# Kernel optimization log

Measured on AMD Instinct MI355X. Metric: run time of the kernel, lower is better.

## Reference

```python
import jax, jax.numpy as jnp
import numpy as np

N_NODES = 100000
N_EDGES = 600000
N_FEAT = 128
N_HID = 128
N_GRAPHS = 256


def gcn_conv(x, src, dst, W, b, n_nodes):
    # PyG GCNConv: h = x @ W; add self-loops; sym-normalize; scatter-add; + bias
    h = x @ W  # [N, H]
    loop = jnp.arange(n_nodes)
    s = jnp.concatenate([src, loop])
    d = jnp.concatenate([dst, loop])
    deg = jax.ops.segment_sum(jnp.ones_like(d, dtype=h.dtype), d, num_segments=n_nodes)
    dinv = jnp.where(deg > 0, jax.lax.rsqrt(deg), 0.0)
    norm = dinv[s] * dinv[d]  # [E+N]
    msg = h[s] * norm[:, None]  # gather + scale
    out = jax.ops.segment_sum(msg, d, num_segments=n_nodes)  # scatter-add
    return out + b


def setup_inputs() -> dict:
    key = jax.random.key(0)
    ks = jax.random.split(key, 12)
    x = jax.random.normal(ks[0], (N_NODES, N_FEAT), dtype=jnp.float32)
    edge_index = jax.random.randint(ks[1], (2, N_EDGES), 0, N_NODES, dtype=jnp.int64)
    batch = jnp.sort(jax.random.randint(ks[2], (N_NODES,), 0, N_GRAPHS, dtype=jnp.int64))
    def lin(k, fi, fo):
        s = 1.0 / np.sqrt(fi)
        return jax.random.uniform(k, (fi, fo), jnp.float32, -s, s)
    params = {
        'W1': lin(ks[3], N_FEAT, N_HID), 'b1': jnp.zeros((N_HID,), jnp.float32),
        'W2': lin(ks[4], N_HID, N_HID), 'b2': jnp.zeros((N_HID,), jnp.float32),
        'W3': lin(ks[5], N_HID, N_HID), 'b3': jnp.zeros((N_HID,), jnp.float32),
        'W4': lin(ks[6], N_HID, N_HID), 'b4': jnp.zeros((N_HID,), jnp.float32),
        'Ws1': lin(ks[7], N_HID, N_HID), 'bs1': jnp.zeros((N_HID,), jnp.float32),
        'Ws2': lin(ks[8], N_HID, 1), 'bs2': jnp.zeros((1,), jnp.float32),
    }
    return {'x': x, 'edge_index': edge_index, 'batch': batch, **params}


def reference(x, edge_index, batch, W1, b1, W2, b2, W3, b3, W4, b4, Ws1, bs1, Ws2, bs2):
    src, dst = edge_index[0], edge_index[1]
    h = x
    # 2 conv blocks = 4 GCNConv layers, each followed by ReLU
    for W, b in ((W1, b1), (W2, b2), (W3, b3), (W4, b4)):
        h = jax.nn.relu(gcn_conv(h, src, dst, W, b, N_NODES))
    # global mean pool over nodes per graph
    sums = jax.ops.segment_sum(h, batch, num_segments=N_GRAPHS)  # [G, H]
    cnt = jax.ops.segment_sum(jnp.ones((h.shape[0],), h.dtype), batch, num_segments=N_GRAPHS)
    pooled = sums / jnp.maximum(cnt, 1.0)[:, None]
    # summary MLP: Linear -> ReLU -> Linear(->1)
    out = jax.nn.relu(pooled @ Ws1 + bs1) @ Ws2 + bs2  # [G, 1]
    return out
```

## Files before the change

kernel.cpp:

```cpp
#include <hip/hip_runtime.h>

#define N_NODES 100000
#define N_EDGES 600000
#define NF 128
#define NG 256

typedef _Float16 f16;
typedef f16 half8 __attribute__((ext_vector_type(8)));
typedef f16 half4v __attribute__((ext_vector_type(4)));
typedef float float4v __attribute__((ext_vector_type(4)));


__global__ void k_count(const int* __restrict__ ei, int* __restrict__ counts) {
    int e = blockIdx.x * 256 + threadIdx.x;
    if (e < N_EDGES) atomicAdd(&counts[ei[N_EDGES + e]], 1);
}

__global__ void k_scan1(const int* __restrict__ counts, int* __restrict__ row_ptr,
                        int* __restrict__ bsums, float* __restrict__ dinv) {
    __shared__ int s[256];
    int b = blockIdx.x, t = threadIdx.x;
    int base = b * 2048 + t * 8;
    int local[8];
    int sum = 0;
#pragma unroll
    for (int q = 0; q < 8; q++) {
        int idx = base + q;
        int v = (idx < N_NODES) ? counts[idx] : 0;
        if (idx < N_NODES) dinv[idx] = 1.0f / sqrtf((float)(v + 1));
        local[q] = sum;
        sum += v;
    }
    s[t] = sum;
    __syncthreads();
    for (int off = 1; off < 256; off <<= 1) {
        int v = 0;
        if (t >= off) v = s[t - off];
        __syncthreads();
        s[t] += v;
        __syncthreads();
    }
    int excl = s[t] - sum;
#pragma unroll
    for (int q = 0; q < 8; q++) {
        int idx = base + q;
        if (idx < N_NODES) row_ptr[idx] = excl + local[q];
    }
    if (t == 255) bsums[b] = s[255];
}

__global__ void k_scan3(int* __restrict__ row_ptr, const int* __restrict__ bsums,
                        int* __restrict__ cursor) {
    __shared__ int pre;
    if (threadIdx.x == 0) {
        int g = blockIdx.x >> 3;
        int s = 0;
        for (int j = 0; j < g; j++) s += bsums[j];
        pre = s;
    }
    __syncthreads();
    int i = blockIdx.x * 256 + threadIdx.x;
    if (i < N_NODES) {
        int v = row_ptr[i] + pre;
        row_ptr[i] = v;
        cursor[i] = v;
        if (i == 0) row_ptr[N_NODES] = N_EDGES;
    }
}

__global__ void k_fill(const int* __restrict__ ei, int* __restrict__ cursor,
                       int* __restrict__ col,
                       const float* __restrict__ W1, const float* __restrict__ W2,
                       const float* __restrict__ W3, const float* __restrict__ W4,
                       f16* __restrict__ wtH) {
    int e = blockIdx.x * 256 + threadIdx.x;
    if (e < N_EDGES) {
        int d = ei[N_EDGES + e];
        int p = atomicAdd(&cursor[d], 1);
        col[p] = ei[e];
    }
    if (blockIdx.x < 256) {
        int idx = blockIdx.x * 256 + threadIdx.x;
        int layer = idx >> 14;
        int rem = idx & 16383;
        int j = rem & 7;
        int lane = (rem >> 3) & 63;
        int chunk = rem >> 9;
        int wave = chunk >> 3;
        int s = (chunk >> 1) & 3;
        int ct = chunk & 1;
        int n = wave * 32 + ct * 16 + (lane & 15);
        int k = s * 32 + (lane >> 4) * 8 + j;
        const float* W = (layer == 0) ? W1 : (layer == 1) ? W2 : (layer == 2) ? W3 : W4;
        wtH[layer * 16384 + rem] = (f16)W[k * NF + n];
    }
}


template <int XIN>
__global__ __launch_bounds__(256) void k_gemm_mfma(
    const float* __restrict__ X, const f16* __restrict__ A,
    const f16* __restrict__ WTH,
    f16* __restrict__ Z, int M) {
    __shared__ __align__(16) f16 As[64 * 136];

    const int t = threadIdx.x;
    const int row0 = blockIdx.x * 64;
    const int wave = t >> 6;
    const int lane = t & 63;
    const int nl = lane & 15;
    const int quad = lane >> 4;

    auto bofs = [&](int s, int ct) {
        return (size_t)((((wave * 8 + s * 2 + ct) * 64) + lane) << 3);
    };

    half8 cbh[2];
    cbh[0] = *(const half8*)(WTH + bofs(0, 0));
    cbh[1] = *(const half8*)(WTH + bofs(0, 1));

    if (XIN) {
#pragma unroll
        for (int q = 0; q < 8; q++) {
            int lin = t + q * 256;
            int r = lin >> 5, c4 = lin & 31;
            float4 v = make_float4(0.f, 0.f, 0.f, 0.f);
            if (row0 + r < M) v = ((const float4*)(X + (size_t)(row0 + r) * NF))[c4];
            half4v hv = {(f16)v.x, (f16)v.y, (f16)v.z, (f16)v.w};
            *(half4v*)&As[r * 136 + c4 * 4] = hv;
        }
    } else {
#pragma unroll
        for (int q = 0; q < 4; q++) {
            int lin = t + q * 256;
            int r = lin >> 4, c8 = lin & 15;
            half8 v = {};
            if (row0 + r < M) v = *(const half8*)(A + (size_t)(row0 + r) * NF + c8 * 8);
            *(half8*)&As[r * 136 + c8 * 8] = v;
        }
    }
    __syncthreads();

    float4v acc[2][4];
#pragma unroll
    for (int ct = 0; ct < 2; ct++)
#pragma unroll
        for (int rt = 0; rt < 4; rt++) acc[ct][rt] = (float4v)0.f;

#pragma unroll
    for (int s = 0; s < 4; s++) {
        half8 nbh[2];
        if (s < 3) {
            nbh[0] = *(const half8*)(WTH + bofs(s + 1, 0));
            nbh[1] = *(const half8*)(WTH + bofs(s + 1, 1));
        }
        half8 fa[4];
#pragma unroll
        for (int rt = 0; rt < 4; rt++)
            fa[rt] = *(half8*)&As[(rt * 16 + nl) * 136 + s * 32 + quad * 8];
#pragma unroll
        for (int ct = 0; ct < 2; ct++)
#pragma unroll
            for (int rt = 0; rt < 4; rt++)
                acc[ct][rt] = __builtin_amdgcn_mfma_f32_16x16x32_f16(fa[rt], cbh[ct], acc[ct][rt], 0, 0, 0);
        if (s < 3) {
            cbh[0] = nbh[0]; cbh[1] = nbh[1];
        }
    }

    __syncthreads();
#pragma unroll
    for (int ct = 0; ct < 2; ct++)
#pragma unroll
        for (int rt = 0; rt < 4; rt++)
#pragma unroll
            for (int r = 0; r < 4; r++)
                As[(rt * 16 + quad * 4 + r) * 136 + wave * 32 + ct * 16 + nl] =
                    (f16)acc[ct][rt][r];
    __syncthreads();
#pragma unroll
    for (int q = 0; q < 4; q++) {
        int lin = t + q * 256;
        int r = lin >> 4, c8 = lin & 15;
        if (row0 + r < M)
            *(half8*)(Z + (size_t)(row0 + r) * NF + c8 * 8) = *(half8*)&As[r * 136 + c8 * 8];
    }
}


#define ACHUNK 4

__global__ __launch_bounds__(256) void k_agg(const f16* __restrict__ z,
                                             const float* __restrict__ dinv,
                                             const int* __restrict__ row_ptr,
                                             const int* __restrict__ col,
                                             const float* __restrict__ bias,
                                             f16* __restrict__ h) {
    const int t = threadIdx.x;
    const int slot = t >> 4;
    const int fl = t & 15;
    const int sbase = (t & 48);
    const int n0 = (blockIdx.x * 16 + slot) * ACHUNK;
    const half8* z8 = (const half8*)z;

    float bb[8];
    {
        float4 b0 = ((const float4*)bias)[fl * 2];
        float4 b1 = ((const float4*)bias)[fl * 2 + 1];
        bb[0] = b0.x; bb[1] = b0.y; bb[2] = b0.z; bb[3] = b0.w;
        bb[4] = b1.x; bb[5] = b1.y; bb[6] = b1.z; bb[7] = b1.w;
    }

    for (int n = n0; n < n0 + ACHUNK && n < N_NODES; n++) {
        const float di = dinv[n];
        const int beg = row_ptr[n];
        const int end = row_ptr[n + 1];

        float acc[8];
        {
            half8 v = z8[(size_t)n * 16 + fl];
            float w = di * di;
#pragma unroll
            for (int j = 0; j < 8; j++) acc[j] = bb[j] + (float)v[j] * w;
        }

        for (int c = beg; c < end; c += 16) {
            int mcnt = end - c; if (mcnt > 16) mcnt = 16;
            int ce = c + fl;
            int colv = (ce < end) ? col[ce] : 0;
            float dvv = dinv[colv];

            int j = 0;
            for (; j + 1 < mcnt; j += 2) {
                int s1 = __shfl(colv, sbase + j, 64);
                float w1 = __shfl(dvv, sbase + j, 64) * di;
                int s2 = __shfl(colv, sbase + j + 1, 64);
                float w2 = __shfl(dvv, sbase + j + 1, 64) * di;
                half8 v1 = z8[(size_t)s1 * 16 + fl];
                half8 v2 = z8[(size_t)s2 * 16 + fl];
#pragma unroll
                for (int q = 0; q < 8; q++) acc[q] += (float)v1[q] * w1;
#pragma unroll
                for (int q = 0; q < 8; q++) acc[q] += (float)v2[q] * w2;
            }
            if (j < mcnt) {
                int s1 = __shfl(colv, sbase + j, 64);
                float w1 = __shfl(dvv, sbase + j, 64) * di;
                half8 v1 = z8[(size_t)s1 * 16 + fl];
#pragma unroll
                for (int q = 0; q < 8; q++) acc[q] += (float)v1[q] * w1;
            }
        }

        half8 o;
#pragma unroll
        for (int j = 0; j < 8; j++) o[j] = (f16)fmaxf(acc[j], 0.f);
        ((half8*)h)[(size_t)n * 16 + fl] = o;
    }
}


__global__ __launch_bounds__(256) void k_agg_gemm(
    const f16* __restrict__ z, const float* __restrict__ dinv,
    const int* __restrict__ row_ptr, const int* __restrict__ col,
    const float* __restrict__ bias,
    const f16* __restrict__ WTH,
    f16* __restrict__ Zout) {
    __shared__ __align__(16) f16 As[64 * 136];

    const int t = threadIdx.x;
    const int slot = t >> 4;
    const int fl = t & 15;
    const int sbase = (t & 48);
    const int n0 = (blockIdx.x * 16 + slot) * ACHUNK;
    const half8* z8 = (const half8*)z;

    float bb[8];
    {
        float4 b0 = ((const float4*)bias)[fl * 2];
        float4 b1 = ((const float4*)bias)[fl * 2 + 1];
        bb[0] = b0.x; bb[1] = b0.y; bb[2] = b0.z; bb[3] = b0.w;
        bb[4] = b1.x; bb[5] = b1.y; bb[6] = b1.z; bb[7] = b1.w;
    }

#pragma unroll 1
    for (int i = 0; i < ACHUNK; i++) {
        const int n = n0 + i;
        half8 o = {};
        if (n < N_NODES) {
            const float di = dinv[n];
            const int beg = row_ptr[n];
            const int end = row_ptr[n + 1];

            float acc[8];
            {
                half8 v = z8[(size_t)n * 16 + fl];
                float w = di * di;
#pragma unroll
                for (int j = 0; j < 8; j++) acc[j] = bb[j] + (float)v[j] * w;
            }

            for (int c = beg; c < end; c += 16) {
                int mcnt = end - c; if (mcnt > 16) mcnt = 16;
                int ce = c + fl;
                int colv = (ce < end) ? col[ce] : 0;
                float dvv = dinv[colv];

                int j = 0;
                for (; j + 1 < mcnt; j += 2) {
                    int s1 = __shfl(colv, sbase + j, 64);
                    float w1 = __shfl(dvv, sbase + j, 64) * di;
                    int s2 = __shfl(colv, sbase + j + 1, 64);
                    float w2 = __shfl(dvv, sbase + j + 1, 64) * di;
                    half8 v1 = z8[(size_t)s1 * 16 + fl];
                    half8 v2 = z8[(size_t)s2 * 16 + fl];
#pragma unroll
                    for (int q = 0; q < 8; q++) acc[q] += (float)v1[q] * w1;
#pragma unroll
                    for (int q = 0; q < 8; q++) acc[q] += (float)v2[q] * w2;
                }
                if (j < mcnt) {
                    int s1 = __shfl(colv, sbase + j, 64);
                    float w1 = __shfl(dvv, sbase + j, 64) * di;
                    half8 v1 = z8[(size_t)s1 * 16 + fl];
#pragma unroll
                    for (int q = 0; q < 8; q++) acc[q] += (float)v1[q] * w1;
                }
            }
#pragma unroll
            for (int j = 0; j < 8; j++) o[j] = (f16)fmaxf(acc[j], 0.f);
        }
        *(half8*)&As[(slot * ACHUNK + i) * 136 + fl * 8] = o;
    }

    const int wave = t >> 6;
    const int lane = t & 63;
    const int nl = lane & 15;
    const int quad = lane >> 4;
    const int row0 = blockIdx.x * 64;

    auto bofs = [&](int s, int ct) {
        return (size_t)((((wave * 8 + s * 2 + ct) * 64) + lane) << 3);
    };

    half8 cbh[2];
    cbh[0] = *(const half8*)(WTH + bofs(0, 0));
    cbh[1] = *(const half8*)(WTH + bofs(0, 1));
    __syncthreads();

    float4v acc[2][4];
#pragma unroll
    for (int ct = 0; ct < 2; ct++)
#pragma unroll
        for (int rt = 0; rt < 4; rt++) acc[ct][rt] = (float4v)0.f;

#pragma unroll
    for (int s = 0; s < 4; s++) {
        half8 nbh[2];
        if (s < 3) {
            nbh[0] = *(const half8*)(WTH + bofs(s + 1, 0));
            nbh[1] = *(const half8*)(WTH + bofs(s + 1, 1));
        }
        half8 fa[4];
#pragma unroll
        for (int rt = 0; rt < 4; rt++)
            fa[rt] = *(half8*)&As[(rt * 16 + nl) * 136 + s * 32 + quad * 8];
#pragma unroll
        for (int ct = 0; ct < 2; ct++)
#pragma unroll
            for (int rt = 0; rt < 4; rt++)
                acc[ct][rt] = __builtin_amdgcn_mfma_f32_16x16x32_f16(fa[rt], cbh[ct], acc[ct][rt], 0, 0, 0);
        if (s < 3) {
            cbh[0] = nbh[0]; cbh[1] = nbh[1];
        }
    }

    __syncthreads();
#pragma unroll
    for (int ct = 0; ct < 2; ct++)
#pragma unroll
        for (int rt = 0; rt < 4; rt++)
#pragma unroll
            for (int r = 0; r < 4; r++)
                As[(rt * 16 + quad * 4 + r) * 136 + wave * 32 + ct * 16 + nl] =
                    (f16)acc[ct][rt][r];
    __syncthreads();
#pragma unroll
    for (int q = 0; q < 4; q++) {
        int lin = t + q * 256;
        int r = lin >> 4, c8 = lin & 15;
        if (row0 + r < N_NODES)
            *(half8*)(Zout + (size_t)(row0 + r) * NF + c8 * 8) = *(half8*)&As[r * 136 + c8 * 8];
    }
}


#define POOL_CHUNK 64

__global__ __launch_bounds__(128) void k_pool2(const f16* __restrict__ h,
                                               const int* __restrict__ batch,
                                               float* __restrict__ pooled) {
    int f = threadIdx.x;
    int n0 = blockIdx.x * POOL_CHUNK;
    int n1 = n0 + POOL_CHUNK;
    if (n1 > N_NODES) n1 = N_NODES;
    if (n0 >= N_NODES) return;
    int g = batch[n0];
    float acc = 0.f;
    for (int n = n0; n < n1; n++) {
        int gn = batch[n];
        if (gn != g) {
            atomicAdd(&pooled[g * NF + f], acc);
            acc = 0.f;
            g = gn;
        }
        acc += (float)h[(size_t)n * NF + f];
    }
    atomicAdd(&pooled[g * NF + f], acc);
}


__global__ void k_mlp(const float* __restrict__ pooled, const int* __restrict__ batch,
                      const float* __restrict__ Ws1, const float* __restrict__ bs1,
                      const float* __restrict__ Ws2, const float* __restrict__ bs2,
                      float* __restrict__ out) {
    __shared__ float row[NF];
    __shared__ float red[NF];
    int g = blockIdx.x, f = threadIdx.x;
    int lo = 0, hi = N_NODES;
    while (lo < hi) { int mid = (lo + hi) >> 1; if (batch[mid] < g) lo = mid + 1; else hi = mid; }
    int start = lo;
    hi = N_NODES;
    while (lo < hi) { int mid = (lo + hi) >> 1; if (batch[mid] < g + 1) lo = mid + 1; else hi = mid; }
    float cnt = (float)(lo - start);
    row[f] = pooled[g * NF + f] / fmaxf(cnt, 1.f);
    __syncthreads();
    float t = bs1[f];
    for (int k = 0; k < NF; k++) t += row[k] * Ws1[k * NF + f];
    t = fmaxf(t, 0.f);
    red[f] = t * Ws2[f];
    __syncthreads();
    for (int s = 64; s > 0; s >>= 1) {
        if (f < s) red[f] += red[f + s];
        __syncthreads();
    }
    if (f == 0) out[g] = red[0] + bs2[0];
}


extern "C" void kernel_launch(void* const* d_in, const int* in_sizes, int n_in,
                              void* d_out, int out_size, void* d_ws, size_t ws_size,
                              hipStream_t stream) {
    const float* x    = (const float*)d_in[0];
    const int*   ei   = (const int*)d_in[1];
    const int*   batch= (const int*)d_in[2];
    const float* W1 = (const float*)d_in[3];  const float* b1 = (const float*)d_in[4];
    const float* W2 = (const float*)d_in[5];  const float* b2 = (const float*)d_in[6];
    const float* W3 = (const float*)d_in[7];  const float* b3 = (const float*)d_in[8];
    const float* W4 = (const float*)d_in[9];  const float* b4 = (const float*)d_in[10];
    const float* Ws1= (const float*)d_in[11]; const float* bs1= (const float*)d_in[12];
    const float* Ws2= (const float*)d_in[13]; const float* bs2= (const float*)d_in[14];
    float* out = (float*)d_out;

    char* ws = (char*)d_ws;
    size_t off = 0;
    auto alloc = [&](size_t bytes) {
        void* p = ws + off;
        off += (bytes + 255) & ~(size_t)255;
        return p;
    };
    f16*   bufA   = (f16*)alloc((size_t)N_NODES * NF * 2);
    f16*   bufB   = (f16*)alloc((size_t)N_NODES * NF * 2);
    f16*   wtH    = (f16*)alloc((size_t)4 * NF * NF * 2);
    int*   counts = (int*)alloc((size_t)N_NODES * 4);
    int*   row_ptr= (int*)alloc((size_t)(N_NODES + 1) * 4);
    int*   cursor = (int*)alloc((size_t)N_NODES * 4);
    int*   col    = (int*)alloc((size_t)N_EDGES * 4);
    int*   bsums  = (int*)alloc(64 * 4);
    float* dinv   = (float*)alloc((size_t)N_NODES * 4);
    float* pooled = (float*)alloc((size_t)NG * NF * 4);

    hipMemsetAsync(counts, 0, (size_t)N_NODES * 4, stream);
    hipMemsetAsync(pooled, 0, (size_t)NG * NF * 4, stream);
    k_count<<<(N_EDGES + 255) / 256, 256, 0, stream>>>(ei, counts);
    int nscan = (N_NODES + 2047) / 2048;
    k_scan1<<<nscan, 256, 0, stream>>>(counts, row_ptr, bsums, dinv);
    k_scan3<<<(N_NODES + 255) / 256, 256, 0, stream>>>(row_ptr, bsums, cursor);
    k_fill<<<(N_EDGES + 255) / 256, 256, 0, stream>>>(ei, cursor, col,
                                                      W1, W2, W3, W4, wtH);

    int gblocks = (N_NODES + 63) / 64;
    int ablocks = (N_NODES + 16 * ACHUNK - 1) / (16 * ACHUNK);

    k_gemm_mfma<1><<<gblocks, 256, 0, stream>>>(x, nullptr, wtH, bufA, N_NODES);
    k_agg_gemm<<<gblocks, 256, 0, stream>>>(bufA, dinv, row_ptr, col, b1,
                                            wtH + 16384, bufB);
    k_agg_gemm<<<gblocks, 256, 0, stream>>>(bufB, dinv, row_ptr, col, b2,
                                            wtH + 32768, bufA);
    k_agg_gemm<<<gblocks, 256, 0, stream>>>(bufA, dinv, row_ptr, col, b3,
                                            wtH + 49152, bufB);
    k_agg<<<ablocks, 256, 0, stream>>>(bufB, dinv, row_ptr, col, b4, bufA);

    int pblocks = (N_NODES + POOL_CHUNK - 1) / POOL_CHUNK;
    k_pool2<<<pblocks, 128, 0, stream>>>(bufA, batch, pooled);
    k_mlp<<<NG, 128, 0, stream>>>(pooled, batch, Ws1, bs1, Ws2, bs2, out);
}
```

Before: 368.5 us.

## Pre-scale GEMM outputs by dinv and interleave two-node neighbor gathers

Folds the source-side dinv factor into the GEMM epilogue, so the aggregation becomes a plain sum of prescaled rows times the destination dinv. This removes the per-edge dinv gather and multiply. The aggregation loop is restructured to prefetch row pointers, self rows and the first column chunk for all four nodes, then processes two nodes at once with up to four outstanding gathers each, raising memory-level parallelism. The cost is more registers and more branchy code, and the output is rounded to fp16 after the dinv scaling.

```diff
diff --git a/kernel.cpp b/kernel.cpp
--- a/kernel.cpp
+++ b/kernel.cpp
@@ -97,12 +97,110 @@
 }
 
 
-template <int XIN>
-__global__ __launch_bounds__(256) void k_gemm_mfma(
-    const float* __restrict__ X, const f16* __restrict__ A,
-    const f16* __restrict__ WTH,
-    f16* __restrict__ Z, int M) {
+__device__ __forceinline__ void agg_tail(const half8* __restrict__ z8,
+                                         const int* __restrict__ col,
+                                         int sbase, int fl, int beg, int end,
+                                         float acc[8]) {
+    for (int c = beg + 16; c < end; c += 16) {
+        int ce = c + fl;
+        int cv = (ce < end) ? col[ce] : 0;
+        int mc = end - c; if (mc > 16) mc = 16;
+        for (int j = 0; j < mc; j += 4) {
+            int kk = mc - j;
+            half8 v0 = {}, v1 = {}, v2 = {}, v3 = {};
+            int s0 = __shfl(cv, sbase + j + 0, 64);
+            v0 = z8[(size_t)s0 * 16 + fl];
+            if (kk > 1) { int s1 = __shfl(cv, sbase + j + 1, 64); v1 = z8[(size_t)s1 * 16 + fl]; }
+            if (kk > 2) { int s2 = __shfl(cv, sbase + j + 2, 64); v2 = z8[(size_t)s2 * 16 + fl]; }
+            if (kk > 3) { int s3 = __shfl(cv, sbase + j + 3, 64); v3 = z8[(size_t)s3 * 16 + fl]; }
+#pragma unroll
+            for (int q = 0; q < 8; q++) acc[q] += (float)v0[q];
+            if (kk > 1) {
+#pragma unroll
+                for (int q = 0; q < 8; q++) acc[q] += (float)v1[q];
+            }
+            if (kk > 2) {
+#pragma unroll
+                for (int q = 0; q < 8; q++) acc[q] += (float)v2[q];
+            }
+            if (kk > 3) {
+#pragma unroll
+                for (int q = 0; q < 8; q++) acc[q] += (float)v3[q];
+            }
+        }
+    }
+}
+
+__device__ __forceinline__ void agg_pair(const half8* __restrict__ z8,
+                                         const int* __restrict__ col,
+                                         int sbase, int fl,
+                                         int begA, int endA, int begB, int endB,
+                                         int colvA, int colvB,
+                                         float accA[8], float accB[8]) {
+    int mA = endA - begA; if (mA > 16) mA = 16;
+    int mB = endB - begB; if (mB > 16) mB = 16;
+    const int mmax = (mA > mB) ? mA : mB;
+    for (int j = 0; j < mmax; j += 4) {
+        const int kA = mA - j, kB = mB - j;
+        half8 vA0 = {}, vA1 = {}, vA2 = {}, vA3 = {};
+        half8 vB0 = {}, vB1 = {}, vB2 = {}, vB3 = {};
+        if (kA > 0) {
+            int s0 = __shfl(colvA, sbase + j + 0, 64);
+            vA0 = z8[(size_t)s0 * 16 + fl];
+            if (kA > 1) { int s1 = __shfl(colvA, sbase + j + 1, 64); vA1 = z8[(size_t)s1 * 16 + fl]; }
+            if (kA > 2) { int s2 = __shfl(colvA, sbase + j + 2, 64); vA2 = z8[(size_t)s2 * 16 + fl]; }
+            if (kA > 3) { int s3 = __shfl(colvA, sbase + j + 3, 64); vA3 = z8[(size_t)s3 * 16 + fl]; }
+        }
+        if (kB > 0) {
+            int s0 = __shfl(colvB, sbase + j + 0, 64);
+            vB0 = z8[(size_t)s0 * 16 + fl];
+            if (kB > 1) { int s1 = __shfl(colvB, sbase + j + 1, 64); vB1 = z8[(size_t)s1 * 16 + fl]; }
+            if (kB > 2) { int s2 = __shfl(colvB, sbase + j + 2, 64); vB2 = z8[(size_t)s2 * 16 + fl]; }
+            if (kB > 3) { int s3 = __shfl(colvB, sbase + j + 3, 64); vB3 = z8[(size_t)s3 * 16 + fl]; }
+        }
+        if (kA > 0) {
+#pragma unroll
+            for (int q = 0; q < 8; q++) accA[q] += (float)vA0[q];
+            if (kA > 1) {
+#pragma unroll
+                for (int q = 0; q < 8; q++) accA[q] += (float)vA1[q];
+            }
+            if (kA > 2) {
+#pragma unroll
+                for (int q = 0; q < 8; q++) accA[q] += (float)vA2[q];
+            }
+            if (kA > 3) {
+#pragma unroll
+                for (int q = 0; q < 8; q++) accA[q] += (float)vA3[q];
+            }
+        }
+        if (kB > 0) {
+#pragma unroll
+            for (int q = 0; q < 8; q++) accB[q] += (float)vB0[q];
+            if (kB > 1) {
+#pragma unroll
+                for (int q = 0; q < 8; q++) accB[q] += (float)vB1[q];
+            }
+            if (kB > 2) {
+#pragma unroll
+                for (int q = 0; q < 8; q++) accB[q] += (float)vB2[q];
+            }
+            if (kB > 3) {
+#pragma unroll
+                for (int q = 0; q < 8; q++) accB[q] += (float)vB3[q];
+            }
+        }
+    }
+    if (endA - begA > 16) agg_tail(z8, col, sbase, fl, begA, endA, accA);
+    if (endB - begB > 16) agg_tail(z8, col, sbase, fl, begB, endB, accB);
+}
+
+
+__global__ __launch_bounds__(256) void k_gemm1(
+    const float* __restrict__ X, const f16* __restrict__ WTH,
+    const float* __restrict__ dinv, f16* __restrict__ Z, int M) {
     __shared__ __align__(16) f16 As[64 * 136];
+    __shared__ float sdi[64];
 
     const int t = threadIdx.x;
     const int row0 = blockIdx.x * 64;
@@ -119,25 +217,15 @@
     cbh[0] = *(const half8*)(WTH + bofs(0, 0));
     cbh[1] = *(const half8*)(WTH + bofs(0, 1));
 
-    if (XIN) {
-#pragma unroll
-        for (int q = 0; q < 8; q++) {
-            int lin = t + q * 256;
-            int r = lin >> 5, c4 = lin & 31;
-            float4 v = make_float4(0.f, 0.f, 0.f, 0.f);
-            if (row0 + r < M) v = ((const float4*)(X + (size_t)(row0 + r) * NF))[c4];
-            half4v hv = {(f16)v.x, (f16)v.y, (f16)v.z, (f16)v.w};
-            *(half4v*)&As[r * 136 + c4 * 4] = hv;
-        }
-    } else {
-#pragma unroll
-        for (int q = 0; q < 4; q++) {
-            int lin = t + q * 256;
-            int r = lin >> 4, c8 = lin & 15;
-            half8 v = {};
-            if (row0 + r < M) v = *(const half8*)(A + (size_t)(row0 + r) * NF + c8 * 8);
-            *(half8*)&As[r * 136 + c8 * 8] = v;
-        }
+    if (t < 64) sdi[t] = (row0 + t < M) ? dinv[row0 + t] : 0.f;
+#pragma unroll
+    for (int q = 0; q < 8; q++) {
+        int lin = t + q * 256;
+        int r = lin >> 5, c4 = lin & 31;
+        float4 v = make_float4(0.f, 0.f, 0.f, 0.f);
+        if (row0 + r < M) v = ((const float4*)(X + (size_t)(row0 + r) * NF))[c4];
+        half4v hv = {(f16)v.x, (f16)v.y, (f16)v.z, (f16)v.w};
+        *(half4v*)&As[r * 136 + c4 * 4] = hv;
     }
     __syncthreads();
 
@@ -176,7 +264,7 @@
 #pragma unroll
             for (int r = 0; r < 4; r++)
                 As[(rt * 16 + quad * 4 + r) * 136 + wave * 32 + ct * 16 + nl] =
-                    (f16)acc[ct][rt][r];
+                    (f16)(acc[ct][rt][r] * sdi[rt * 16 + quad * 4 + r]);
     __syncthreads();
 #pragma unroll
     for (int q = 0; q < 4; q++) {
@@ -189,6 +277,135 @@
 
 
 #define ACHUNK 4
+
+__global__ __launch_bounds__(256) void k_agg_gemm(
+    const f16* __restrict__ z, const float* __restrict__ dinv,
+    const int* __restrict__ row_ptr, const int* __restrict__ col,
+    const float* __restrict__ bias,
+    const f16* __restrict__ WTH,
+    f16* __restrict__ Zout) {
+    __shared__ __align__(16) f16 As[64 * 136];
+    __shared__ float sdi[64];
+
+    const int t = threadIdx.x;
+    const int slot = t >> 4;
+    const int fl = t & 15;
+    const int sbase = (t & 48);
+    const int n0 = (blockIdx.x * 16 + slot) * ACHUNK;
+    const half8* z8 = (const half8*)z;
+
+    float bb[8];
+    {
+        float4 b0 = ((const float4*)bias)[fl * 2];
+        float4 b1 = ((const float4*)bias)[fl * 2 + 1];
+        bb[0] = b0.x; bb[1] = b0.y; bb[2] = b0.z; bb[3] = b0.w;
+        bb[4] = b1.x; bb[5] = b1.y; bb[6] = b1.z; bb[7] = b1.w;
+    }
+
+    int rp[5];
+#pragma unroll
+    for (int i = 0; i < 5; i++) {
+        int n = n0 + i;
+        rp[i] = row_ptr[(n < N_NODES) ? n : N_NODES];
+    }
+    float dis[4]; half8 selfv[4]; int colv0[4];
+#pragma unroll
+    for (int i = 0; i < 4; i++) {
+        int n = n0 + i;
+        bool ok = n < N_NODES;
+        half8 zz = {};
+        dis[i] = ok ? dinv[n] : 0.f;
+        selfv[i] = ok ? z8[(size_t)n * 16 + fl] : zz;
+        int ce = rp[i] + fl;
+        colv0[i] = (ce < rp[i + 1]) ? col[ce] : 0;
+    }
+    if (fl == 0) {
+#pragma unroll
+        for (int i = 0; i < 4; i++) sdi[slot * ACHUNK + i] = dis[i];
+    }
+
+#pragma unroll
+    for (int p = 0; p < 2; p++) {
+        const int iA = 2 * p, iB = 2 * p + 1;
+        float accA[8], accB[8];
+#pragma unroll
+        for (int q = 0; q < 8; q++) {
+            accA[q] = (float)selfv[iA][q];
+            accB[q] = (float)selfv[iB][q];
+        }
+        agg_pair(z8, col, sbase, fl, rp[iA], rp[iA + 1], rp[iB], rp[iB + 1],
+                 colv0[iA], colv0[iB], accA, accB);
+        half8 oA, oB;
+#pragma unroll
+        for (int q = 0; q < 8; q++) {
+            oA[q] = (f16)fmaxf(bb[q] + dis[iA] * accA[q], 0.f);
+            oB[q] = (f16)fmaxf(bb[q] + dis[iB] * accB[q], 0.f);
+        }
+        *(half8*)&As[(slot * ACHUNK + iA) * 136 + fl * 8] = oA;
+        *(half8*)&As[(slot * ACHUNK + iB) * 136 + fl * 8] = oB;
+    }
+
+    const int wave = t >> 6;
+    const int lane = t & 63;
+    const int nl = lane & 15;
+    const int quad = lane >> 4;
+    const int row0 = blockIdx.x * 64;
+
+    auto bofs = [&](int s, int ct) {
+        return (size_t)((((wave * 8 + s * 2 + ct) * 64) + lane) << 3);
+    };
+
+    half8 cbh[2];
+    cbh[0] = *(const half8*)(WTH + bofs(0, 0));
+    cbh[1] = *(const half8*)(WTH + bofs(0, 1));
+    __syncthreads();
+
+    float4v acc[2][4];
+#pragma unroll
+    for (int ct = 0; ct < 2; ct++)
+#pragma unroll
+        for (int rt = 0; rt < 4; rt++) acc[ct][rt] = (float4v)0.f;
+
+#pragma unroll
+    for (int s = 0; s < 4; s++) {
+        half8 nbh[2];
+        if (s < 3) {
+            nbh[0] = *(const half8*)(WTH + bofs(s + 1, 0));
+            nbh[1] = *(const half8*)(WTH + bofs(s + 1, 1));
+        }
+        half8 fa[4];
+#pragma unroll
+        for (int rt = 0; rt < 4; rt++)
+            fa[rt] = *(half8*)&As[(rt * 16 + nl) * 136 + s * 32 + quad * 8];
+#pragma unroll
+        for (int ct = 0; ct < 2; ct++)
+#pragma unroll
+            for (int rt = 0; rt < 4; rt++)
+                acc[ct][rt] = __builtin_amdgcn_mfma_f32_16x16x32_f16(fa[rt], cbh[ct], acc[ct][rt], 0, 0, 0);
+        if (s < 3) {
+            cbh[0] = nbh[0]; cbh[1] = nbh[1];
+        }
+    }
+
+    __syncthreads();
+#pragma unroll
+    for (int ct = 0; ct < 2; ct++)
+#pragma unroll
+        for (int rt = 0; rt < 4; rt++)
+#pragma unroll
+            for (int r = 0; r < 4; r++)
+                As[(rt * 16 + quad * 4 + r) * 136 + wave * 32 + ct * 16 + nl] =
+                    (f16)(acc[ct][rt][r] * sdi[rt * 16 + quad * 4 + r]);
+    __syncthreads();
+#pragma unroll
+    for (int q = 0; q < 4; q++) {
+        int lin = t + q * 256;
+        int r = lin >> 4, c8 = lin & 15;
+        if (row0 + r < N_NODES)
+            *(half8*)(Zout + (size_t)(row0 + r) * NF + c8 * 8) = *(half8*)&As[r * 136 + c8 * 8];
+    }
+}
+
 
 __global__ __launch_bounds__(256) void k_agg(const f16* __restrict__ z,
                                              const float* __restrict__ dinv,
@@ -211,186 +428,43 @@
         bb[4] = b1.x; bb[5] = b1.y; bb[6] = b1.z; bb[7] = b1.w;
     }
 
-    for (int n = n0; n < n0 + ACHUNK && n < N_NODES; n++) {
-        const float di = dinv[n];
-        const int beg = row_ptr[n];
-        const int end = row_ptr[n + 1];
-
-        float acc[8];
-        {
-            half8 v = z8[(size_t)n * 16 + fl];
-            float w = di * di;
-#pragma unroll
-            for (int j = 0; j < 8; j++) acc[j] = bb[j] + (float)v[j] * w;
-        }
-
-        for (int c = beg; c < end; c += 16) {
-            int mcnt = end - c; if (mcnt > 16) mcnt = 16;
-            int ce = c + fl;
-            int colv = (ce < end) ? col[ce] : 0;
-            float dvv = dinv[colv];
-
-            int j = 0;
-            for (; j + 1 < mcnt; j += 2) {
-                int s1 = __shfl(colv, sbase + j, 64);
-                float w1 = __shfl(dvv, sbase + j, 64) * di;
-                int s2 = __shfl(colv, sbase + j + 1, 64);
-                float w2 = __shfl(dvv, sbase + j + 1, 64) * di;
-                half8 v1 = z8[(size_t)s1 * 16 + fl];
-                half8 v2 = z8[(size_t)s2 * 16 + fl];
-#pragma unroll
-                for (int q = 0; q < 8; q++) acc[q] += (float)v1[q] * w1;
-#pragma unroll
-                for (int q = 0; q < 8; q++) acc[q] += (float)v2[q] * w2;
-            }
-            if (j < mcnt) {
-                int s1 = __shfl(colv, sbase + j, 64);
-                float w1 = __shfl(dvv, sbase + j, 64) * di;
-                half8 v1 = z8[(size_t)s1 * 16 + fl];
-#pragma unroll
-                for (int q = 0; q < 8; q++) acc[q] += (float)v1[q] * w1;
-            }
-        }
-
-        half8 o;
-#pragma unroll
-        for (int j = 0; j < 8; j++) o[j] = (f16)fmaxf(acc[j], 0.f);
-        ((half8*)h)[(size_t)n * 16 + fl] = o;
-    }
-}
-
-
-__global__ __launch_bounds__(256) void k_agg_gemm(
-    const f16* __restrict__ z, const float* __restrict__ dinv,
-    const int* __restrict__ row_ptr, const int* __restrict__ col,
-    const float* __restrict__ bias,
-    const f16* __restrict__ WTH,
-    f16* __restrict__ Zout) {
-    __shared__ __align__(16) f16 As[64 * 136];
-
-    const int t = threadIdx.x;
-    const int slot = t >> 4;
-    const int fl = t & 15;
-    const int sbase = (t & 48);
-    const int n0 = (blockIdx.x * 16 + slot) * ACHUNK;
-    const half8* z8 = (const half8*)z;
-
-    float bb[8];
-    {
-        float4 b0 = ((const float4*)bias)[fl * 2];
-        float4 b1 = ((const float4*)bias)[fl * 2 + 1];
-        bb[0] = b0.x; bb[1] = b0.y; bb[2] = b0.z; bb[3] = b0.w;
-        bb[4] = b1.x; bb[5] = b1.y; bb[6] = b1.z; bb[7] = b1.w;
-    }
-
-#pragma unroll 1
-    for (int i = 0; i < ACHUNK; i++) {
-        const int n = n0 + i;
-        half8 o = {};
-        if (n < N_NODES) {
-            const float di = dinv[n];
-            const int beg = row_ptr[n];
-            const int end = row_ptr[n + 1];
-
-            float acc[8];
-            {
-                half8 v = z8[(size_t)n * 16 + fl];
-                float w = di * di;
-#pragma unroll
-                for (int j = 0; j < 8; j++) acc[j] = bb[j] + (float)v[j] * w;
-            }
-
-            for (int c = beg; c < end; c += 16) {
-                int mcnt = end - c; if (mcnt > 16) mcnt = 16;
-                int ce = c + fl;
-                int colv = (ce < end) ? col[ce] : 0;
-                float dvv = dinv[colv];
-
-                int j = 0;
-                for (; j + 1 < mcnt; j += 2) {
-                    int s1 = __shfl(colv, sbase + j, 64);
-                    float w1 = __shfl(dvv, sbase + j, 64) * di;
-                    int s2 = __shfl(colv, sbase + j + 1, 64);
-                    float w2 = __shfl(dvv, sbase + j + 1, 64) * di;
-                    half8 v1 = z8[(size_t)s1 * 16 + fl];
-                    half8 v2 = z8[(size_t)s2 * 16 + fl];
-#pragma unroll
-                    for (int q = 0; q < 8; q++) acc[q] += (float)v1[q] * w1;
-#pragma unroll
-                    for (int q = 0; q < 8; q++) acc[q] += (float)v2[q] * w2;
-                }
-                if (j < mcnt) {
-                    int s1 = __shfl(colv, sbase + j, 64);
-                    float w1 = __shfl(dvv, sbase + j, 64) * di;
-                    half8 v1 = z8[(size_t)s1 * 16 + fl];
-#pragma unroll
-                    for (int q = 0; q < 8; q++) acc[q] += (float)v1[q] * w1;
-                }
-            }
-#pragma unroll
-            for (int j = 0; j < 8; j++) o[j] = (f16)fmaxf(acc[j], 0.f);
-        }
-        *(half8*)&As[(slot * ACHUNK + i) * 136 + fl * 8] = o;
-    }
-
-    const int wave = t >> 6;
-    const int lane = t & 63;
-    const int nl = lane & 15;
-    const int quad = lane >> 4;
-    const int row0 = blockIdx.x * 64;
-
-    auto bofs = [&](int s, int ct) {
-        return (size_t)((((wave * 8 + s * 2 + ct) * 64) + lane) << 3);
-    };
-
-    half8 cbh[2];
-    cbh[0] = *(const half8*)(WTH + bofs(0, 0));
-    cbh[1] = *(const half8*)(WTH + bofs(0, 1));
-    __syncthreads();
-
-    float4v acc[2][4];
-#pragma unroll
-    for (int ct = 0; ct < 2; ct++)
-#pragma unroll
-        for (int rt = 0; rt < 4; rt++) acc[ct][rt] = (float4v)0.f;
-
-#pragma unroll
-    for (int s = 0; s < 4; s++) {
-        half8 nbh[2];
-        if (s < 3) {
-            nbh[0] = *(const half8*)(WTH + bofs(s + 1, 0));
-            nbh[1] = *(const half8*)(WTH + bofs(s + 1, 1));
-        }
-        half8 fa[4];
-#pragma unroll
-        for (int rt = 0; rt < 4; rt++)
-            fa[rt] = *(half8*)&As[(rt * 16 + nl) * 136 + s * 32 + quad * 8];
-#pragma unroll
-        for (int ct = 0; ct < 2; ct++)
-#pragma unroll
-            for (int rt = 0; rt < 4; rt++)
-                acc[ct][rt] = __builtin_amdgcn_mfma_f32_16x16x32_f16(fa[rt], cbh[ct], acc[ct][rt], 0, 0, 0);
-        if (s < 3) {
-            cbh[0] = nbh[0]; cbh[1] = nbh[1];
-        }
-    }
-
-    __syncthreads();
-#pragma unroll
-    for (int ct = 0; ct < 2; ct++)
-#pragma unroll
-        for (int rt = 0; rt < 4; rt++)
-#pragma unroll
-            for (int r = 0; r < 4; r++)
-                As[(rt * 16 + quad * 4 + r) * 136 + wave * 32 + ct * 16 + nl] =
-                    (f16)acc[ct][rt][r];
-    __syncthreads();
-#pragma unroll
-    for (int q = 0; q < 4; q++) {
-        int lin = t + q * 256;
-        int r = lin >> 4, c8 = lin & 15;
-        if (row0 + r < N_NODES)
-            *(half8*)(Zout + (size_t)(row0 + r) * NF + c8 * 8) = *(half8*)&As[r * 136 + c8 * 8];
+    int rp[5];
+#pragma unroll
+    for (int i = 0; i < 5; i++) {
+        int n = n0 + i;
+        rp[i] = row_ptr[(n < N_NODES) ? n : N_NODES];
+    }
+    float dis[4]; half8 selfv[4]; int colv0[4];
+#pragma unroll
+    for (int i = 0; i < 4; i++) {
+        int n = n0 + i;
+        bool ok = n < N_NODES;
+        half8 zz = {};
+        dis[i] = ok ? dinv[n] : 0.f;
+        selfv[i] = ok ? z8[(size_t)n * 16 + fl] : zz;
+        int ce = rp[i] + fl;
+        colv0[i] = (ce < rp[i + 1]) ? col[ce] : 0;
+    }
+
+#pragma unroll
+    for (int p = 0; p < 2; p++) {
+        const int iA = 2 * p, iB = 2 * p + 1;
+        float accA[8], accB[8];
+#pragma unroll
+        for (int q = 0; q < 8; q++) {
+            accA[q] = (float)selfv[iA][q];
+            accB[q] = (float)selfv[iB][q];
+        }
+        agg_pair(z8, col, sbase, fl, rp[iA], rp[iA + 1], rp[iB], rp[iB + 1],
+                 colv0[iA], colv0[iB], accA, accB);
+        half8 oA, oB;
+#pragma unroll
+        for (int q = 0; q < 8; q++) {
+            oA[q] = (f16)fmaxf(bb[q] + dis[iA] * accA[q], 0.f);
+            oB[q] = (f16)fmaxf(bb[q] + dis[iB] * accB[q], 0.f);
+        }
+        if (n0 + iA < N_NODES) ((half8*)h)[(size_t)(n0 + iA) * 16 + fl] = oA;
+        if (n0 + iB < N_NODES) ((half8*)h)[(size_t)(n0 + iB) * 16 + fl] = oB;
     }
 }
 
@@ -492,7 +566,7 @@
     int gblocks = (N_NODES + 63) / 64;
     int ablocks = (N_NODES + 16 * ACHUNK - 1) / (16 * ACHUNK);
 
-    k_gemm_mfma<1><<<gblocks, 256, 0, stream>>>(x, nullptr, wtH, bufA, N_NODES);
+    k_gemm1<<<gblocks, 256, 0, stream>>>(x, wtH, dinv, bufA, N_NODES);
     k_agg_gemm<<<gblocks, 256, 0, stream>>>(bufA, dinv, row_ptr, col, b1,
                                             wtH + 16384, bufB);
     k_agg_gemm<<<gblocks, 256, 0, stream>>>(bufB, dinv, row_ptr, col, b2,
```

New measurement: 371.0 us. Within noise of the previous version (+0.7%).
